# Kernel tuning notes

Hardware: AMD Instinct MI355X
Metric: run time of the kernel (lower is better)

The kernel has to match this reference:

```python
import jax, jax.numpy as jnp
import numpy as np

B, T, E, H = 4, 2048, 1024, 16
HS = E // H  # 64
EPS = 1e-5


def _layernorm(x, g, b):
    mu = jnp.mean(x, axis=-1, keepdims=True)
    var = jnp.mean(jnp.square(x - mu), axis=-1, keepdims=True)
    return (x - mu) * jax.lax.rsqrt(var + EPS) * g + b


def setup_inputs() -> dict:
    key = jax.random.key(0)
    ks = jax.random.split(key, 12)
    s = 0.02
    return {
        "x": jax.random.normal(ks[0], (B, T, E), dtype=jnp.float32),
        "ln1_g": jnp.ones((E,), jnp.float32),
        "ln1_b": jnp.zeros((E,), jnp.float32),
        "Wq": jax.random.normal(ks[1], (H, E, HS), jnp.float32) * s,
        "Wk": jax.random.normal(ks[2], (H, E, HS), jnp.float32) * s,
        "Wv": jax.random.normal(ks[3], (H, E, HS), jnp.float32) * s,
        "Wo": jax.random.normal(ks[4], (E, E), jnp.float32) * s,
        "bo": jnp.zeros((E,), jnp.float32),
        "ln2_g": jnp.ones((E,), jnp.float32),
        "ln2_b": jnp.zeros((E,), jnp.float32),
        "W1": jax.random.normal(ks[5], (E, 4 * E), jnp.float32) * s,
        "b1": jnp.zeros((4 * E,), jnp.float32),
        "W2": jax.random.normal(ks[6], (4 * E, E), jnp.float32) * s,
        "b2": jnp.zeros((E,), jnp.float32),
    }


def reference(x, ln1_g, ln1_b, Wq, Wk, Wv, Wo, bo, ln2_g, ln2_b, W1, b1, W2, b2):
    # --- self-attention (pre-LN) ---
    h = _layernorm(x, ln1_g, ln1_b)                      # [B,T,E]
    q = jnp.einsum('bte,hed->bhtd', h, Wq)               # [B,H,T,HS]
    k = jnp.einsum('bte,hed->bhtd', h, Wk)
    v = jnp.einsum('bte,hed->bhtd', h, Wv)
    scores = jnp.einsum('bhtd,bhsd->bhts', q, k) * (HS ** -0.5)  # [B,H,T,T]
    att = jax.nn.softmax(scores, axis=-1)
    o = jnp.einsum('bhts,bhsd->bhtd', att, v)            # [B,H,T,HS]
    o = jnp.transpose(o, (0, 2, 1, 3)).reshape(B, T, E)  # concat heads
    x = x + o @ Wo + bo                                  # residual
    # --- feed-forward (pre-LN) ---
    h2 = _layernorm(x, ln2_g, ln2_b)
    x = x + jax.nn.relu(h2 @ W1 + b1) @ W2 + b2
    return x
```

## Files before the change

kernel.cpp:

```cpp
#include <hip/hip_runtime.h>
#include <stdint.h>


typedef __attribute__((ext_vector_type(8))) short s16x8;
typedef __attribute__((ext_vector_type(4))) float f32x4;
typedef unsigned short u16;
typedef __attribute__((ext_vector_type(4))) unsigned short u16x4;

#define XSW(r) ((((r) & 7) ^ (((r) >> 3) & 7)) << 4)

__device__ __forceinline__ u16 f2bf(float f) {
    uint32_t u = __float_as_uint(f);
    u += 0x7fffu + ((u >> 16) & 1u);
    return (u16)(u >> 16);
}
__device__ __forceinline__ float bf2f(u16 u) {
    return __uint_as_float(((uint32_t)u) << 16);
}
__device__ __forceinline__ uint32_t pk2(float a, float b) {
    return (uint32_t)f2bf(a) | ((uint32_t)f2bf(b) << 16);
}
__device__ __forceinline__ float exp2_fast(float x) {
    float r;
    asm("v_exp_f32 %0, %1" : "=v"(r) : "v"(x));
    return r;
}

__device__ __forceinline__ void gld16(const void* g, void* l) {
    __builtin_amdgcn_global_load_lds(
        (const __attribute__((address_space(1))) unsigned int*)g,
        (__attribute__((address_space(3))) unsigned int*)l, 16, 0, 0);
}

__global__ __launch_bounds__(256)
void ln_bf16(const float* __restrict__ x, const float* __restrict__ g,
             const float* __restrict__ bta, u16* __restrict__ y) {
    __shared__ float red[8];
    const int row = blockIdx.x;
    const int t = threadIdx.x;
    const float4 xv = ((const float4*)(x + (size_t)row * 1024))[t];
    float s = xv.x + xv.y + xv.z + xv.w;
    float q = xv.x*xv.x + xv.y*xv.y + xv.z*xv.z + xv.w*xv.w;
#pragma unroll
    for (int off = 32; off; off >>= 1) {
        s += __shfl_down(s, off, 64);
        q += __shfl_down(q, off, 64);
    }
    if ((t & 63) == 0) { red[(t>>6)*2] = s; red[(t>>6)*2+1] = q; }
    __syncthreads();
    const float st = red[0]+red[2]+red[4]+red[6];
    const float qt = red[1]+red[3]+red[5]+red[7];
    const float mu = st * (1.f/1024.f);
    const float rs = rsqrtf(qt*(1.f/1024.f) - mu*mu + 1e-5f);
    const float4 gv = ((const float4*)g)[t];
    const float4 bv = ((const float4*)bta)[t];
    u16x4 o;
    o.x = f2bf((xv.x-mu)*rs*gv.x + bv.x);
    o.y = f2bf((xv.y-mu)*rs*gv.y + bv.y);
    o.z = f2bf((xv.z-mu)*rs*gv.z + bv.z);
    o.w = f2bf((xv.w-mu)*rs*gv.w + bv.w);
    ((u16x4*)(y + (size_t)row*1024))[t] = o;
}

__global__ __launch_bounds__(256)
void transpose_f32_bf16(const float* __restrict__ in, u16* __restrict__ out,
                        int K, int N) {
    __shared__ float tile[64][65];
    const int k0 = blockIdx.x * 64;
    const int n0 = blockIdx.y * 64;
    const int t = threadIdx.x;
    const int r = t >> 2;
    const int c = (t & 3) * 16;
    const float* ip = in + (size_t)(k0 + r) * N + n0 + c;
#pragma unroll
    for (int i = 0; i < 4; ++i) {
        const float4 v = *(const float4*)(ip + i*4);
        tile[r][c+i*4+0]=v.x; tile[r][c+i*4+1]=v.y;
        tile[r][c+i*4+2]=v.z; tile[r][c+i*4+3]=v.w;
    }
    __syncthreads();
    u16 tmp[16] __attribute__((aligned(16)));
#pragma unroll
    for (int i = 0; i < 16; ++i) tmp[i] = f2bf(tile[c+i][r]);
    u16* op = out + (size_t)(n0 + r) * K + k0 + c;
    *(s16x8*)op       = *(const s16x8*)&tmp[0];
    *(s16x8*)(op + 8) = *(const s16x8*)&tmp[8];
}

__global__ __launch_bounds__(256)
void pack_wcat(const float* __restrict__ Wq, const float* __restrict__ Wk,
               const float* __restrict__ Wv, u16* __restrict__ out) {
    __shared__ float tile[64][65];
    const int ph = blockIdx.y;
    const int p = ph >> 4, h = ph & 15;
    const float* W = (p == 0) ? Wq : (p == 1 ? Wk : Wv);
    const float* in = W + (size_t)h * 64 * 1024;
    const int k0 = blockIdx.x * 64;
    const int t = threadIdx.x;
    const int r = t >> 2;
    const int c = (t & 3) * 16;
    const float* ip = in + (size_t)(k0 + r) * 64 + c;
#pragma unroll
    for (int i = 0; i < 4; ++i) {
        const float4 v = *(const float4*)(ip + i*4);
        tile[r][c+i*4+0]=v.x; tile[r][c+i*4+1]=v.y;
        tile[r][c+i*4+2]=v.z; tile[r][c+i*4+3]=v.w;
    }
    __syncthreads();
    u16 tmp[16] __attribute__((aligned(16)));
#pragma unroll
    for (int i = 0; i < 16; ++i) tmp[i] = f2bf(tile[c+i][r]);
    u16* op = out + (size_t)(p*1024 + h*64 + r) * 1024 + k0 + c;
    *(s16x8*)op       = *(const s16x8*)&tmp[0];
    *(s16x8*)(op + 8) = *(const s16x8*)&tmp[8];
}

template<bool RELU, bool HAS_BIAS, bool HAS_RES, bool OUT_BF16, bool SPLIT_V>
__global__ __launch_bounds__(256)
void bgemm(const u16* __restrict__ A, int lda,
           const u16* __restrict__ Bt, int ldb,
           void* Cv, int ldc,
           const float* __restrict__ bias,
           const float* Res, int ldres, int K,
           u16* __restrict__ vT)
{
    __shared__ u16 Als[128*64];
    __shared__ u16 Bls[128*64];
    const int tid = threadIdx.x;
    const int wid = tid >> 6, lane = tid & 63;
    const int bm = blockIdx.y * 128, bn = blockIdx.x * 128;
    const int wr = (wid >> 1) * 64, wc = (wid & 1) * 64;
    const int fr = lane & 15, fq = lane >> 4;
    const int sr8 = lane >> 3, sc8 = (lane & 7) * 8;

    const f32x4 zero = {0.f, 0.f, 0.f, 0.f};
    f32x4 acc[4][4];
#pragma unroll
    for (int m = 0; m < 4; ++m)
#pragma unroll
        for (int n = 0; n < 4; ++n) acc[m][n] = zero;

    const u16* Ap = A  + (size_t)(bm + wid*32 + sr8) * lda + sc8;
    const u16* Bp = Bt + (size_t)(bn + wid*32 + sr8) * ldb + sc8;
    u16* Alp = Als + wid*2048 + lane*8;
    u16* Blp = Bls + wid*2048 + lane*8;

    for (int k0 = 0; k0 < K; k0 += 64) {
#pragma unroll
        for (int c = 0; c < 4; ++c) {
            gld16(Ap + (size_t)(c*8)*lda + k0, Alp + c*512);
            gld16(Bp + (size_t)(c*8)*ldb + k0, Blp + c*512);
        }
        __syncthreads();
#pragma unroll
        for (int kk = 0; kk < 2; ++kk) {
            s16x8 af[4], bf[4];
#pragma unroll
            for (int m = 0; m < 4; ++m)
                af[m] = *(const s16x8*)((const char*)Als + (wr+m*16+fr)*128 + kk*64 + fq*16);
#pragma unroll
            for (int n = 0; n < 4; ++n)
                bf[n] = *(const s16x8*)((const char*)Bls + (wc+n*16+fr)*128 + kk*64 + fq*16);
#pragma unroll
            for (int m = 0; m < 4; ++m)
#pragma unroll
                for (int n = 0; n < 4; ++n)
                    acc[m][n] = __builtin_amdgcn_mfma_f32_16x16x32_bf16(
                        af[m], bf[n], acc[m][n], 0, 0, 0);
        }
        __syncthreads();
    }

    float* Cf = (float*)Cv;
    u16*  Cb = (u16*)Cv;
    if (SPLIT_V && bn >= 2048) {
#pragma unroll
        for (int n = 0; n < 4; ++n) {
            const int local = bn + wc + n*16 + fr - 2048;
            const int hh = local >> 6, dd = local & 63;
#pragma unroll
            for (int m = 0; m < 4; ++m) {
#pragma unroll
                for (int j = 0; j < 4; ++j) {
                    const int row = bm + wr + m*16 + fq*4 + j;
                    const int bb = row >> 11, tt = row & 2047;
                    vT[((size_t)(bb*16 + hh)*64 + dd)*2048 + tt] = f2bf(acc[m][n][j]);
                }
            }
        }
        return;
    }
#pragma unroll
    for (int n = 0; n < 4; ++n) {
        const int col = bn + wc + n*16 + fr;
        const float bval = HAS_BIAS ? bias[col] : 0.f;
#pragma unroll
        for (int m = 0; m < 4; ++m) {
#pragma unroll
            for (int j = 0; j < 4; ++j) {
                const int row = bm + wr + m*16 + fq*4 + j;
                float v = acc[m][n][j] + bval;
                if (HAS_RES) v += Res[(size_t)row * ldres + col];
                if (RELU)    v = fmaxf(v, 0.f);
                if (OUT_BF16) Cb[(size_t)row * ldc + col] = f2bf(v);
                else          Cf[(size_t)row * ldc + col] = v;
            }
        }
    }
}

__global__ __launch_bounds__(256)
void attn_bf16(const u16* __restrict__ qk, const u16* __restrict__ vT,
               u16* __restrict__ out) {
    __shared__ u16 Ks[128*64];
    __shared__ u16 Vt[64*128];
    __shared__ u16 Ps[4][16*128];
    const int b = blockIdx.y >> 4, h = blockIdx.y & 15;
    const int q0 = blockIdx.x << 6;
    const int tid = threadIdx.x;
    const int wid = tid >> 6, lane = tid & 63;
    const int fr = lane & 15, fq = lane >> 4;
    const int srow = tid >> 2;
    const int sce  = (tid & 3) * 16;
    const int vd   = tid >> 4;
    const int vt0  = (tid & 15) * 8;
    const size_t tokbase = (size_t)b * 2048;
    const u16* vbase = vT + (size_t)(b*16 + h) * 64 * 2048;
    const f32x4 zero = {0.f, 0.f, 0.f, 0.f};

    u16* Qst = (u16*)Ps;
    {
        const u16* qp = qk + (tokbase + q0 + srow)*2048 + h*64 + sce;
        const s16x8 v0 = *(const s16x8*)qp;
        const s16x8 v1 = *(const s16x8*)(qp + 8);
        *(s16x8*)((char*)Qst + srow*128 + ((sce*2)      ^ XSW(srow))) = v0;
        *(s16x8*)((char*)Qst + srow*128 + ((sce*2 + 16) ^ XSW(srow))) = v1;
    }
    __syncthreads();
    s16x8 qf[2];
    {
        const int qrow = wid*16 + fr;
        const float qscale = 0.125f * 1.44269504f;
#pragma unroll
        for (int kk = 0; kk < 2; ++kk) {
            const s16x8 raw = *(const s16x8*)((const char*)Qst + qrow*128
                                 + ((kk*64 + fq*16) ^ XSW(qrow)));
#pragma unroll
            for (int i = 0; i < 8; ++i)
                qf[kk][i] = (short)f2bf(bf2f((u16)raw[i]) * qscale);
        }
    }

    float m_run = -1e30f, l_run = 0.f;
    f32x4 oacc[4];
#pragma unroll
    for (int nd = 0; nd < 4; ++nd) oacc[nd] = zero;

    s16x8 kr[4], vr[4];
    {
        const u16* kp0 = qk + (tokbase + srow)*2048 + 1024 + h*64 + sce;
        kr[0] = *(const s16x8*)kp0;
        kr[1] = *(const s16x8*)(kp0 + 8);
        kr[2] = *(const s16x8*)(kp0 + (size_t)64*2048);
        kr[3] = *(const s16x8*)(kp0 + (size_t)64*2048 + 8);
#pragma unroll
        for (int c = 0; c < 4; ++c)
            vr[c] = *(const s16x8*)(vbase + (size_t)(vd + 16*c)*2048 + vt0);
    }

    for (int kt = 0; kt < 2048; kt += 128) {
        __syncthreads();
        {
            const int r0 = srow, r1 = srow + 64;
            *(s16x8*)((char*)Ks + r0*128 + ((sce*2)      ^ XSW(r0))) = kr[0];
            *(s16x8*)((char*)Ks + r0*128 + ((sce*2 + 16) ^ XSW(r0))) = kr[1];
            *(s16x8*)((char*)Ks + r1*128 + ((sce*2)      ^ XSW(r1))) = kr[2];
            *(s16x8*)((char*)Ks + r1*128 + ((sce*2 + 16) ^ XSW(r1))) = kr[3];
        }
#pragma unroll
        for (int c = 0; c < 4; ++c) {
            const int d = vd + 16*c;
            *(s16x8*)((char*)Vt + d*256 + ((vt0*2) ^ XSW(d))) = vr[c];
        }
        __syncthreads();

        if (kt + 128 < 2048) {
            const u16* kp0 = qk + (tokbase + kt + 128 + srow)*2048 + 1024 + h*64 + sce;
            kr[0] = *(const s16x8*)kp0;
            kr[1] = *(const s16x8*)(kp0 + 8);
            kr[2] = *(const s16x8*)(kp0 + (size_t)64*2048);
            kr[3] = *(const s16x8*)(kp0 + (size_t)64*2048 + 8);
#pragma unroll
            for (int c = 0; c < 4; ++c)
                vr[c] = *(const s16x8*)(vbase + (size_t)(vd + 16*c)*2048
                                        + kt + 128 + vt0);
        }

        f32x4 sv[8];
        __builtin_amdgcn_s_setprio(1);
#pragma unroll
        for (int n = 0; n < 8; ++n) {
            sv[n] = zero;
            const int r = n*16 + fr;
#pragma unroll
            for (int kk = 0; kk < 2; ++kk) {
                const s16x8 kf = *(const s16x8*)((const char*)Ks + r*128
                                     + ((kk*64 + fq*16) ^ XSW(r)));
                sv[n] = __builtin_amdgcn_mfma_f32_16x16x32_bf16(kf, qf[kk], sv[n], 0,0,0);
            }
        }
        __builtin_amdgcn_s_setprio(0);

        float pv[32];
        float mx = -1e30f;
#pragma unroll
        for (int n = 0; n < 8; ++n)
#pragma unroll
            for (int j = 0; j < 4; ++j) {
                const float s = sv[n][j];
                pv[n*4 + j] = s;
                mx = fmaxf(mx, s);
            }
        mx = fmaxf(mx, __shfl_xor(mx, 16, 64));
        mx = fmaxf(mx, __shfl_xor(mx, 32, 64));
        const float mn = fmaxf(m_run, mx);
        const float al = exp2_fast(m_run - mn);
        m_run = mn;
        float rs = 0.f;
#pragma unroll
        for (int t = 0; t < 32; ++t) { pv[t] = exp2_fast(pv[t] - mn); rs += pv[t]; }
        rs += __shfl_xor(rs, 16, 64);
        rs += __shfl_xor(rs, 32, 64);
        l_run = l_run * al + rs;
#pragma unroll
        for (int nd = 0; nd < 4; ++nd)
#pragma unroll
            for (int j = 0; j < 4; ++j) oacc[nd][j] *= al;

        u16* Pw = (u16*)Ps + wid*2048;
#pragma unroll
        for (int n = 0; n < 8; ++n) {
            const uint64_t w = (uint64_t)pk2(pv[n*4+0], pv[n*4+1])
                             | ((uint64_t)pk2(pv[n*4+2], pv[n*4+3]) << 32);
            *(uint64_t*)((char*)Pw + fr*256 + ((n*32 + fq*8) ^ XSW(fr))) = w;
        }
        asm volatile("s_waitcnt lgkmcnt(0)" ::: "memory");
        __builtin_amdgcn_sched_barrier(0);

        s16x8 pf[4];
#pragma unroll
        for (int k2 = 0; k2 < 4; ++k2)
            pf[k2] = *(const s16x8*)((const char*)Pw + fr*256
                         + ((k2*64 + fq*16) ^ XSW(fr)));
        __builtin_amdgcn_s_setprio(1);
#pragma unroll
        for (int nd = 0; nd < 4; ++nd) {
            const int d = nd*16 + fr;
#pragma unroll
            for (int k2 = 0; k2 < 4; ++k2) {
                const s16x8 vf = *(const s16x8*)((const char*)Vt + d*256
                                     + ((k2*64 + fq*16) ^ XSW(d)));
                oacc[nd] = __builtin_amdgcn_mfma_f32_16x16x32_bf16(vf, pf[k2], oacc[nd], 0,0,0);
            }
        }
        __builtin_amdgcn_s_setprio(0);
    }

    const float inv = 1.0f / l_run;
    const size_t row = tokbase + q0 + wid*16 + fr;
#pragma unroll
    for (int nd = 0; nd < 4; ++nd) {
        u16x4 o;
#pragma unroll
        for (int j = 0; j < 4; ++j) o[j] = f2bf(oacc[nd][j] * inv);
        *(u16x4*)(out + row*1024 + h*64 + nd*16 + fq*4) = o;
    }
}

extern "C" void kernel_launch(void* const* d_in, const int* in_sizes, int n_in,
                              void* d_out, int out_size, void* d_ws, size_t ws_size,
                              hipStream_t stream) {
    (void)in_sizes; (void)n_in; (void)out_size; (void)ws_size;
    const float* x     = (const float*)d_in[0];
    const float* ln1_g = (const float*)d_in[1];
    const float* ln1_b = (const float*)d_in[2];
    const float* Wq    = (const float*)d_in[3];
    const float* Wk    = (const float*)d_in[4];
    const float* Wv    = (const float*)d_in[5];
    const float* Wo    = (const float*)d_in[6];
    const float* bo    = (const float*)d_in[7];
    const float* ln2_g = (const float*)d_in[8];
    const float* ln2_b = (const float*)d_in[9];
    const float* W1    = (const float*)d_in[10];
    const float* b1    = (const float*)d_in[11];
    const float* W2    = (const float*)d_in[12];
    const float* b2    = (const float*)d_in[13];
    float* out = (float*)d_out;

    char* w = (char*)d_ws;
    u16* WcatT = (u16*)w;  w += (size_t)3072*1024*2;
    u16* WoT   = (u16*)w;  w += (size_t)1024*1024*2;
    u16* W1T   = (u16*)w;  w += (size_t)4096*1024*2;
    u16* W2T   = (u16*)w;  w += (size_t)1024*4096*2;
    u16* hb    = (u16*)w;  w += (size_t)8192*1024*2;
    u16* qkb   = (u16*)w;  w += (size_t)8192*2048*2;
    u16* vTb   = (u16*)w;  w += (size_t)64*64*2048*2;
    u16* attno = (u16*)w;  w += (size_t)8192*1024*2;
    u16* a1    = (u16*)w;  w += (size_t)8192*4096*2;

    pack_wcat<<<dim3(16, 48), 256, 0, stream>>>(Wq, Wk, Wv, WcatT);
    transpose_f32_bf16<<<dim3(16, 16), 256, 0, stream>>>(Wo, WoT, 1024, 1024);
    transpose_f32_bf16<<<dim3(16, 64), 256, 0, stream>>>(W1, W1T, 1024, 4096);
    transpose_f32_bf16<<<dim3(64, 16), 256, 0, stream>>>(W2, W2T, 4096, 1024);

    ln_bf16<<<dim3(8192), 256, 0, stream>>>(x, ln1_g, ln1_b, hb);
    bgemm<false,false,false,true,true><<<dim3(24, 64), 256, 0, stream>>>(
        hb, 1024, WcatT, 1024, qkb, 2048, nullptr, nullptr, 0, 1024, vTb);
    attn_bf16<<<dim3(32, 64), 256, 0, stream>>>(qkb, vTb, attno);
    bgemm<false,true,true,false,false><<<dim3(8, 64), 256, 0, stream>>>(
        attno, 1024, WoT, 1024, out, 1024, bo, x, 1024, 1024, nullptr);
    ln_bf16<<<dim3(8192), 256, 0, stream>>>(out, ln2_g, ln2_b, hb);
    bgemm<true,true,false,true,false><<<dim3(32, 64), 256, 0, stream>>>(
        hb, 1024, W1T, 1024, a1, 4096, b1, nullptr, 0, 1024, nullptr);
    bgemm<false,true,true,false,false><<<dim3(8, 64), 256, 0, stream>>>(
        a1, 4096, W2T, 4096, out, 1024, b2, out, 1024, 4096, nullptr);
}
```

Measured before the change: 640.5 us.

## Replace GEMM with 256x256 double-buffered tiles, swizzled LDS, and packed bf16 conversion

The 128x128 single-buffer GEMM is replaced with a 512-thread, 256x256-tile kernel. It double-buffers LDS so the next K-tile's global-to-LDS loads overlap compute, XOR-swizzles the LDS layout to avoid bank conflicts, and remaps workgroups for L2 locality. Separately, software float-to-bf16 rounding is replaced with the hardware v_cvt_pk_bf16_f32 instruction in layernorm and attention. Risks: 128 KB of LDS and 128 accumulator registers per thread limit occupancy, and the larger tiles give fewer workgroups for the N=1024 GEMMs (128 blocks).

New measurement: 701.0 us. 1.09x slower.

```diff
diff --git a/kernel.cpp b/kernel.cpp
--- a/kernel.cpp
+++ b/kernel.cpp
@@ -17,8 +17,10 @@
 __device__ __forceinline__ float bf2f(u16 u) {
     return __uint_as_float(((uint32_t)u) << 16);
 }
-__device__ __forceinline__ uint32_t pk2(float a, float b) {
-    return (uint32_t)f2bf(a) | ((uint32_t)f2bf(b) << 16);
+__device__ __forceinline__ uint32_t cvtpk(float a, float b) {
+    uint32_t r;
+    asm("v_cvt_pk_bf16_f32 %0, %1, %2" : "=v"(r) : "v"(a), "v"(b));
+    return r;
 }
 __device__ __forceinline__ float exp2_fast(float x) {
     float r;
@@ -54,12 +56,10 @@
     const float rs = rsqrtf(qt*(1.f/1024.f) - mu*mu + 1e-5f);
     const float4 gv = ((const float4*)g)[t];
     const float4 bv = ((const float4*)bta)[t];
-    u16x4 o;
-    o.x = f2bf((xv.x-mu)*rs*gv.x + bv.x);
-    o.y = f2bf((xv.y-mu)*rs*gv.y + bv.y);
-    o.z = f2bf((xv.z-mu)*rs*gv.z + bv.z);
-    o.w = f2bf((xv.w-mu)*rs*gv.w + bv.w);
-    ((u16x4*)(y + (size_t)row*1024))[t] = o;
+    uint2 o;
+    o.x = cvtpk((xv.x-mu)*rs*gv.x + bv.x, (xv.y-mu)*rs*gv.y + bv.y);
+    o.y = cvtpk((xv.z-mu)*rs*gv.z + bv.z, (xv.w-mu)*rs*gv.w + bv.w);
+    ((uint2*)(y + (size_t)row*1024))[t] = o;
 }
 
 __global__ __launch_bounds__(256)
@@ -116,90 +116,118 @@
 }
 
 template<bool RELU, bool HAS_BIAS, bool HAS_RES, bool OUT_BF16, bool SPLIT_V>
-__global__ __launch_bounds__(256)
-void bgemm(const u16* __restrict__ A, int lda,
-           const u16* __restrict__ Bt, int ldb,
-           void* Cv, int ldc,
-           const float* __restrict__ bias,
-           const float* Res, int ldres, int K,
-           u16* __restrict__ vT)
+__global__ __launch_bounds__(512, 2)
+void bgemm256(const u16* __restrict__ A, int lda,
+              const u16* __restrict__ Bt, int ldb,
+              void* Cv, int ldc,
+              const float* __restrict__ bias,
+              const float* Res, int ldres, int K,
+              u16* __restrict__ vT)
 {
-    __shared__ u16 Als[128*64];
-    __shared__ u16 Bls[128*64];
+    __shared__ u16 As[2][256*64];
+    __shared__ u16 Bs[2][256*64];
     const int tid = threadIdx.x;
     const int wid = tid >> 6, lane = tid & 63;
-    const int bm = blockIdx.y * 128, bn = blockIdx.x * 128;
-    const int wr = (wid >> 1) * 64, wc = (wid & 1) * 64;
+    const int wm = wid >> 2, wn = wid & 3;
     const int fr = lane & 15, fq = lane >> 4;
-    const int sr8 = lane >> 3, sc8 = (lane & 7) * 8;
+    const int nwg = gridDim.x * gridDim.y;
+    const int lin = blockIdx.y * gridDim.x + blockIdx.x;
+    const int swz = (lin & 7) * (nwg >> 3) + (lin >> 3);
+    const int bn = (swz % gridDim.x) * 256;
+    const int bm = (swz / gridDim.x) * 256;
+
+    const int srow8 = lane >> 3;
+    const int sblk  = lane & 7;
 
     const f32x4 zero = {0.f, 0.f, 0.f, 0.f};
-    f32x4 acc[4][4];
-#pragma unroll
-    for (int m = 0; m < 4; ++m)
+    f32x4 acc[8][4];
+#pragma unroll
+    for (int m = 0; m < 8; ++m)
 #pragma unroll
         for (int n = 0; n < 4; ++n) acc[m][n] = zero;
 
-    const u16* Ap = A  + (size_t)(bm + wid*32 + sr8) * lda + sc8;
-    const u16* Bp = Bt + (size_t)(bn + wid*32 + sr8) * ldb + sc8;
-    u16* Alp = Als + wid*2048 + lane*8;
-    u16* Blp = Bls + wid*2048 + lane*8;
-
-    for (int k0 = 0; k0 < K; k0 += 64) {
-#pragma unroll
-        for (int c = 0; c < 4; ++c) {
-            gld16(Ap + (size_t)(c*8)*lda + k0, Alp + c*512);
-            gld16(Bp + (size_t)(c*8)*ldb + k0, Blp + c*512);
-        }
+    const int nt = K >> 6;
+
+    auto STAGE = [&](int u, int d) {
+#pragma unroll
+        for (int q = 0; q < 4; ++q) {
+            const int row = q*64 + wid*8 + srow8;
+            const int blk = sblk ^ (row & 7);
+            gld16(A  + (size_t)(bm + row)*lda + u*64 + blk*8,
+                  &As[d][(q*64 + wid*8)*64]);
+            gld16(Bt + (size_t)(bn + row)*ldb + u*64 + blk*8,
+                  &Bs[d][(q*64 + wid*8)*64]);
+        }
+    };
+
+    STAGE(0, 0);
+    for (int u = 0; u < nt; ++u) {
+        const int c = u & 1;
         __syncthreads();
-#pragma unroll
-        for (int kk = 0; kk < 2; ++kk) {
-            s16x8 af[4], bf[4];
+        if (u + 1 < nt) STAGE(u + 1, c ^ 1);
+#pragma unroll
+        for (int p = 0; p < 4; ++p) {
+            const int mh = p & 1, nh = p >> 1;
+            s16x8 af[4][2], bf[2][2];
+#pragma unroll
+            for (int m = 0; m < 4; ++m) {
+                const int row = wm*128 + mh*64 + m*16 + fr;
+#pragma unroll
+                for (int kk = 0; kk < 2; ++kk)
+                    af[m][kk] = *(const s16x8*)
+                        &As[c][row*64 + (((kk*4 + fq) ^ (row & 7))*8)];
+            }
+#pragma unroll
+            for (int n = 0; n < 2; ++n) {
+                const int row = wn*64 + nh*32 + n*16 + fr;
+#pragma unroll
+                for (int kk = 0; kk < 2; ++kk)
+                    bf[n][kk] = *(const s16x8*)
+                        &Bs[c][row*64 + (((kk*4 + fq) ^ (row & 7))*8)];
+            }
+            __builtin_amdgcn_s_setprio(1);
 #pragma unroll
             for (int m = 0; m < 4; ++m)
-                af[m] = *(const s16x8*)((const char*)Als + (wr+m*16+fr)*128 + kk*64 + fq*16);
-#pragma unroll
-            for (int n = 0; n < 4; ++n)
-                bf[n] = *(const s16x8*)((const char*)Bls + (wc+n*16+fr)*128 + kk*64 + fq*16);
-#pragma unroll
-            for (int m = 0; m < 4; ++m)
-#pragma unroll
-                for (int n = 0; n < 4; ++n)
-                    acc[m][n] = __builtin_amdgcn_mfma_f32_16x16x32_bf16(
-                        af[m], bf[n], acc[m][n], 0, 0, 0);
-        }
-        __syncthreads();
+#pragma unroll
+                for (int n = 0; n < 2; ++n)
+#pragma unroll
+                    for (int kk = 0; kk < 2; ++kk)
+                        acc[mh*4+m][nh*2+n] = __builtin_amdgcn_mfma_f32_16x16x32_bf16(
+                            af[m][kk], bf[n][kk], acc[mh*4+m][nh*2+n], 0, 0, 0);
+            __builtin_amdgcn_s_setprio(0);
+            if (p < 3) __builtin_amdgcn_s_barrier();
+        }
     }
 
     float* Cf = (float*)Cv;
     u16*  Cb = (u16*)Cv;
     if (SPLIT_V && bn >= 2048) {
 #pragma unroll
-        for (int n = 0; n < 4; ++n) {
-            const int local = bn + wc + n*16 + fr - 2048;
+        for (int an = 0; an < 4; ++an) {
+            const int local = bn + wn*64 + (an>>1)*32 + (an&1)*16 + fr - 2048;
             const int hh = local >> 6, dd = local & 63;
 #pragma unroll
-            for (int m = 0; m < 4; ++m) {
+            for (int am = 0; am < 8; ++am) {
 #pragma unroll
                 for (int j = 0; j < 4; ++j) {
-                    const int row = bm + wr + m*16 + fq*4 + j;
+                    const int row = bm + wm*128 + (am>>2)*64 + (am&3)*16 + fq*4 + j;
                     const int bb = row >> 11, tt = row & 2047;
-                    vT[((size_t)(bb*16 + hh)*64 + dd)*2048 + tt] = f2bf(acc[m][n][j]);
+                    vT[((size_t)(bb*16 + hh)*64 + dd)*2048 + tt] = f2bf(acc[am][an][j]);
                 }
             }
         }
         return;
     }
 #pragma unroll
-    for (int n = 0; n < 4; ++n) {
-        const int col = bn + wc + n*16 + fr;
+    for (int an = 0; an < 4; ++an) {
+        const int col = bn + wn*64 + (an>>1)*32 + (an&1)*16 + fr;
         const float bval = HAS_BIAS ? bias[col] : 0.f;
 #pragma unroll
-        for (int m = 0; m < 4; ++m) {
+        for (int am = 0; am < 8; ++am) {
 #pragma unroll
             for (int j = 0; j < 4; ++j) {
-                const int row = bm + wr + m*16 + fq*4 + j;
-                float v = acc[m][n][j] + bval;
+                const int row = bm + wm*128 + (am>>2)*64 + (am&3)*16 + fq*4 + j;
+                float v = acc[am][an][j] + bval;
                 if (HAS_RES) v += Res[(size_t)row * ldres + col];
                 if (RELU)    v = fmaxf(v, 0.f);
                 if (OUT_BF16) Cb[(size_t)row * ldc + col] = f2bf(v);
@@ -240,14 +268,16 @@
     s16x8 qf[2];
     {
         const int qrow = wid*16 + fr;
-        const float qscale = 0.125f * 1.44269504f;
+        const float qs = 0.125f * 1.44269504f;
 #pragma unroll
         for (int kk = 0; kk < 2; ++kk) {
             const s16x8 raw = *(const s16x8*)((const char*)Qst + qrow*128
                                  + ((kk*64 + fq*16) ^ XSW(qrow)));
-#pragma unroll
-            for (int i = 0; i < 8; ++i)
-                qf[kk][i] = (short)f2bf(bf2f((u16)raw[i]) * qscale);
+            union { s16x8 v; uint32_t w[4]; } u;
+#pragma unroll
+            for (int i = 0; i < 4; ++i)
+                u.w[i] = cvtpk(bf2f((u16)raw[2*i])*qs, bf2f((u16)raw[2*i+1])*qs);
+            qf[kk] = u.v;
         }
     }
 
@@ -340,8 +370,8 @@
         u16* Pw = (u16*)Ps + wid*2048;
 #pragma unroll
         for (int n = 0; n < 8; ++n) {
-            const uint64_t w = (uint64_t)pk2(pv[n*4+0], pv[n*4+1])
-                             | ((uint64_t)pk2(pv[n*4+2], pv[n*4+3]) << 32);
+            const uint64_t w = (uint64_t)cvtpk(pv[n*4+0], pv[n*4+1])
+                             | ((uint64_t)cvtpk(pv[n*4+2], pv[n*4+3]) << 32);
             *(uint64_t*)((char*)Pw + fr*256 + ((n*32 + fq*8) ^ XSW(fr))) = w;
         }
         asm volatile("s_waitcnt lgkmcnt(0)" ::: "memory");
@@ -370,10 +400,10 @@
     const size_t row = tokbase + q0 + wid*16 + fr;
 #pragma unroll
     for (int nd = 0; nd < 4; ++nd) {
-        u16x4 o;
-#pragma unroll
-        for (int j = 0; j < 4; ++j) o[j] = f2bf(oacc[nd][j] * inv);
-        *(u16x4*)(out + row*1024 + h*64 + nd*16 + fq*4) = o;
+        uint2 o;
+        o.x = cvtpk(oacc[nd][0]*inv, oacc[nd][1]*inv);
+        o.y = cvtpk(oacc[nd][2]*inv, oacc[nd][3]*inv);
+        *(uint2*)(out + row*1024 + h*64 + nd*16 + fq*4) = o;
     }
 }
 
@@ -414,14 +444,14 @@
     transpose_f32_bf16<<<dim3(64, 16), 256, 0, stream>>>(W2, W2T, 4096, 1024);
 
     ln_bf16<<<dim3(8192), 256, 0, stream>>>(x, ln1_g, ln1_b, hb);
-    bgemm<false,false,false,true,true><<<dim3(24, 64), 256, 0, stream>>>(
+    bgemm256<false,false,false,true,true><<<dim3(12, 32), 512, 0, stream>>>(
         hb, 1024, WcatT, 1024, qkb, 2048, nullptr, nullptr, 0, 1024, vTb);
     attn_bf16<<<dim3(32, 64), 256, 0, stream>>>(qkb, vTb, attno);
-    bgemm<false,true,true,false,false><<<dim3(8, 64), 256, 0, stream>>>(
+    bgemm256<false,true,true,false,false><<<dim3(4, 32), 512, 0, stream>>>(
         attno, 1024, WoT, 1024, out, 1024, bo, x, 1024, 1024, nullptr);
     ln_bf16<<<dim3(8192), 256, 0, stream>>>(out, ln2_g, ln2_b, hb);
-    bgemm<true,true,false,true,false><<<dim3(32, 64), 256, 0, stream>>>(
+    bgemm256<true,true,false,true,false><<<dim3(16, 32), 512, 0, stream>>>(
         hb, 1024, W1T, 1024, a1, 4096, b1, nullptr, 0, 1024, nullptr);
-    bgemm<false,true,true,false,false><<<dim3(8, 64), 256, 0, stream>>>(
+    bgemm256<false,true,true,false,false><<<dim3(4, 32), 512, 0, stream>>>(
         a1, 4096, W2T, 4096, out, 1024, b2, out, 1024, 4096, nullptr);
 }
```
